# Optimization experiments

Hardware: AMD Instinct MI355X
Metric: run time of the kernel (lower is better)

The kernel has to match this reference:

```python
import jax, jax.numpy as jnp
import numpy as np

WD, WH, WW = 2, 7, 7
N = WD * WH * WW          # 98 tokens per window
DIM = 128
HEADS = 4
HEAD_DIM = DIM // HEADS   # 32
B_ = 2048                 # num_windows * batch
NW = 64                   # windows per image (mask leading dim)
TABLE = (2 * WD - 1) * (2 * WH - 1) * (2 * WW - 1)  # 507


def _relative_position_index():
    coords = np.stack(np.meshgrid(np.arange(WD), np.arange(WH), np.arange(WW), indexing='ij'))
    flat = coords.reshape(3, -1)                     # [3, N]
    rel = flat[:, :, None] - flat[:, None, :]        # [3, N, N]
    rel = rel.transpose(1, 2, 0).copy()              # [N, N, 3]
    rel[:, :, 0] += WD - 1
    rel[:, :, 1] += WH - 1
    rel[:, :, 2] += WW - 1
    rel[:, :, 0] *= (2 * WH - 1) * (2 * WW - 1)
    rel[:, :, 1] *= 2 * WW - 1
    return rel.sum(-1).astype(np.int32)             # [N, N]


def setup_inputs() -> dict:
    key = jax.random.key(0)
    ks = jax.random.split(key, 6)
    x = jax.random.normal(ks[0], (B_, N, DIM), dtype=jnp.float32)
    mask = jax.random.normal(ks[1], (NW, N, N), dtype=jnp.float32)
    qkv_w = jax.random.normal(ks[2], (3 * DIM, DIM), dtype=jnp.float32) * 0.02
    qkv_b = jnp.zeros((3 * DIM,), dtype=jnp.float32)
    proj_w = jax.random.normal(ks[3], (DIM, DIM), dtype=jnp.float32) * 0.02
    proj_b = jnp.zeros((DIM,), dtype=jnp.float32)
    bias_table = jax.random.normal(ks[4], (TABLE, HEADS), dtype=jnp.float32) * 0.02
    rel_idx = jnp.asarray(_relative_position_index())
    return {"x": x, "mask": mask, "qkv_w": qkv_w, "qkv_b": qkv_b,
            "proj_w": proj_w, "proj_b": proj_b, "bias_table": bias_table,
            "rel_idx": rel_idx}


def reference(x, mask, qkv_w, qkv_b, proj_w, proj_b, bias_table, rel_idx):
    b, n, c = x.shape
    hd = c // HEADS
    scale = hd ** -0.5
    qkv = x @ qkv_w.T + qkv_b                          # [B_, N, 3C]
    qkv = qkv.reshape(b, n, 3, HEADS, hd)
    qkv = jnp.transpose(qkv, (2, 0, 3, 1, 4))          # [3, B_, H, N, hd]
    q, k, v = qkv[0], qkv[1], qkv[2]
    attn = jnp.einsum('bhnd,bhmd->bhnm', q * scale, k)  # [B_, H, N, N]
    # gathered relative position bias
    bias = bias_table[rel_idx.reshape(-1)].reshape(n, n, HEADS)
    bias = jnp.transpose(bias, (2, 0, 1))               # [H, N, N]
    attn = attn + bias[None]
    nw = mask.shape[0]
    attn = attn.reshape(b // nw, nw, HEADS, n, n) + mask[None, :, None]
    attn = jax.nn.softmax(attn.reshape(b, HEADS, n, n), axis=-1)
    out = jnp.einsum('bhnm,bhmd->bnhd', attn, v).reshape(b, n, c)
    out = out @ proj_w.T + proj_b
    return out
```

## Files before the change

kernel.cpp:

```cpp
#include <hip/hip_runtime.h>
#include <stdint.h>

#define NTOK 98
#define DIM 128
#define HEADS 4
#define HD 32
#define BWIN 2048
#define NW 64
#define SCALE 0.17677669529663687f
#define QSTR 32
#define VSTR 104

typedef __bf16 bf16_t;
typedef bf16_t bf16x8 __attribute__((ext_vector_type(8)));
typedef float f32x4 __attribute__((ext_vector_type(4)));
typedef unsigned short u16;
typedef unsigned int u32;
typedef unsigned long long u64;

__device__ __forceinline__ u16 f2bf(float f) {
    union { bf16_t h; u16 u; } v; v.h = (bf16_t)f; return v.u;
}
__device__ __forceinline__ float bf2f(u16 b) {
    union { u16 u; bf16_t h; } v; v.u = b; return (float)v.h;
}
__device__ __forceinline__ int qk_idx(int row, int d) {
    return row * QSTR + ((((d >> 3) ^ (row & 3)) << 3) | (d & 7));
}

__global__ void k0_prep(const float* __restrict__ qkv_w, const float* __restrict__ proj_w,
                        const float* __restrict__ mask,
                        const float* __restrict__ bias_table, const int* __restrict__ rel_idx,
                        const float* __restrict__ x,
                        u16* __restrict__ qkvw_bf, u16* __restrict__ pw_bf,
                        u16* __restrict__ mbT, u16* __restrict__ xbf)
{
    int t = blockIdx.x * 256 + threadIdx.x;
    if (t < 49152) {
        qkvw_bf[t] = f2bf(qkv_w[t]);
    } else if (t < 65536) {
        int r = t - 49152;
        pw_bf[r] = f2bf(proj_w[r]);
    } else if (t < 3276800) {
        int r = t - 65536;
        int w    = r / 50176;
        int rem  = r - w * 50176;
        int hh   = rem / 12544;
        int rem2 = rem - hh * 12544;
        int i    = rem2 >> 7;
        int c    = rem2 & 127;
        int l16  = c >> 3;
        int njp  = c & 7;
        int j    = njp * 16 + l16;
        float val = 0.f;
        if (njp < 7 && j < NTOK)
            val = mask[w * 9604 + i * NTOK + j] + bias_table[rel_idx[i * NTOK + j] * HEADS + hh];
        mbT[r] = f2bf(val);
    } else if (t < 6488064) {
        size_t idx = (size_t)(t - 3276800) * 8;
        const float4 a0 = *reinterpret_cast<const float4*>(x + idx);
        const float4 a1 = *reinterpret_cast<const float4*>(x + idx + 4);
        u64 p0 = (u64)f2bf(a0.x) | ((u64)f2bf(a0.y) << 16) |
                 ((u64)f2bf(a0.z) << 32) | ((u64)f2bf(a0.w) << 48);
        u64 p1 = (u64)f2bf(a1.x) | ((u64)f2bf(a1.y) << 16) |
                 ((u64)f2bf(a1.z) << 32) | ((u64)f2bf(a1.w) << 48);
        *reinterpret_cast<u64*>(&xbf[idx])     = p0;
        *reinterpret_cast<u64*>(&xbf[idx + 4]) = p1;
    }
}

__global__ __launch_bounds__(256, 5) void k_attn(
    const u16* __restrict__ xbf, const u16* __restrict__ qkvw_bf,
    const float* __restrict__ qkv_b, const u16* __restrict__ mbT,
    u16* __restrict__ OG)
{
    __shared__ __align__(16) u16 qL[NTOK * QSTR];
    __shared__ __align__(16) u16 kL[NTOK * QSTR];
    __shared__ __align__(16) u16 vL[HD * VSTR];
    __shared__ __align__(16) u16 Pscr[4][16 * VSTR];

    const int bh   = (blockIdx.x & 7) * 1024 + (blockIdx.x >> 3);
    const int b    = bh >> 2;
    const int h    = bh & 3;
    const int tid  = threadIdx.x;
    const int wave = tid >> 6;
    const int lane = tid & 63;
    const int l16  = lane & 15;
    const int quad = lane >> 4;

    const u16* xb = xbf + (size_t)b * (NTOK * DIM);

    {
        const int u0 = (wave * 21) >> 2;
        const int u1 = ((wave + 1) * 21) >> 2;
        int cached = -1;
        bf16x8 Bf[2][4];
        float  cb[2];
        for (int u = u0; u < u1; ++u) {
            const int part = u / 7;
            const int mt   = u - part * 7;
            if (part != cached) {
                const u16* wp = qkvw_bf + (size_t)part * DIM * DIM;
#pragma unroll
                for (int nt2 = 0; nt2 < 2; ++nt2) {
                    const int col = h * HD + nt2 * 16 + l16;
#pragma unroll
                    for (int ks = 0; ks < 4; ++ks)
                        Bf[nt2][ks] = *reinterpret_cast<const bf16x8*>(
                            wp + col * DIM + quad * 8 + ks * 32);
                    cb[nt2] = qkv_b[part * DIM + col];
                }
                cached = part;
            }
            int arow = mt * 16 + l16;
            if (arow > 97) arow = 97;
            bf16x8 af[4];
#pragma unroll
            for (int ks = 0; ks < 4; ++ks)
                af[ks] = *reinterpret_cast<const bf16x8*>(
                    xb + arow * DIM + quad * 8 + ks * 32);
            f32x4 acc0 = {0.f, 0.f, 0.f, 0.f};
            f32x4 acc1 = {0.f, 0.f, 0.f, 0.f};
#pragma unroll
            for (int ks = 0; ks < 4; ++ks) {
                acc0 = __builtin_amdgcn_mfma_f32_16x16x32_bf16(af[ks], Bf[0][ks], acc0, 0, 0, 0);
                acc1 = __builtin_amdgcn_mfma_f32_16x16x32_bf16(af[ks], Bf[1][ks], acc1, 0, 0, 0);
            }
            const int tokb = mt * 16 + quad * 4;
#pragma unroll
            for (int nt2 = 0; nt2 < 2; ++nt2) {
                const f32x4& acc = nt2 ? acc1 : acc0;
                const int d = nt2 * 16 + l16;
                const float cbv = cb[nt2];
                if (part == 0) {
#pragma unroll
                    for (int reg = 0; reg < 4; ++reg) {
                        int tok = tokb + reg;
                        if (tok < NTOK)
                            qL[qk_idx(tok, d)] = f2bf((acc[reg] + cbv) * SCALE);
                    }
                } else if (part == 1) {
#pragma unroll
                    for (int reg = 0; reg < 4; ++reg) {
                        int tok = tokb + reg;
                        if (tok < NTOK)
                            kL[qk_idx(tok, d)] = f2bf(acc[reg] + cbv);
                    }
                } else {
                    u16* vrow = &vL[d * VSTR];
                    if (tokb + 3 <= 97) {
                        u64 pack = 0;
#pragma unroll
                        for (int reg = 0; reg < 4; ++reg)
                            pack |= ((u64)f2bf(acc[reg] + cbv)) << (16 * reg);
                        *reinterpret_cast<u64*>(&vrow[tokb]) = pack;
                    } else if (tokb <= 97) {
                        u32 pack = (u32)f2bf(acc[0] + cbv) | ((u32)f2bf(acc[1] + cbv) << 16);
                        *reinterpret_cast<u32*>(&vrow[tokb]) = pack;
                    }
                }
            }
        }
    }
    __syncthreads();

    {
        const u16* mbtp = mbT + ((size_t)((b & (NW - 1)) * HEADS + h)) * (NTOK * 128);
        u16* ps = &Pscr[wave][0];
        const int qko = ((quad ^ (l16 & 3)) << 3);

        bf16x8 kf[7];
#pragma unroll
        for (int nj = 0; nj < 7; ++nj)
            kf[nj] = *reinterpret_cast<const bf16x8*>(&kL[(nj * 16 + l16) * QSTR + qko]);

        for (int mi = 0; mi < 2; ++mi) {
            const int mt = wave + mi * 4;
            if (mt > 6) break;
            bf16x8 mrows[4];
#pragma unroll
            for (int reg = 0; reg < 4; ++reg) {
                int i  = mt * 16 + quad * 4 + reg;
                int ic = (i > 97) ? 97 : i;
                mrows[reg] = *reinterpret_cast<const bf16x8*>(&mbtp[ic * 128 + l16 * 8]);
            }
            bf16x8 qf = *reinterpret_cast<const bf16x8*>(&qL[(mt * 16 + l16) * QSTR + qko]);
            f32x4 sacc[7];
#pragma unroll
            for (int nj = 0; nj < 7; ++nj) {
                f32x4 z = {0.f, 0.f, 0.f, 0.f};
                sacc[nj] = __builtin_amdgcn_mfma_f32_16x16x32_bf16(qf, kf[nj], z, 0, 0, 0);
            }
#pragma unroll
            for (int reg = 0; reg < 4; ++reg) {
                int i = mt * 16 + quad * 4 + reg;
                bool irow = (i < NTOK);
                float s[7];
#pragma unroll
                for (int nj = 0; nj < 7; ++nj) {
                    int j = nj * 16 + l16;
                    float val = -1e30f;
                    if (irow && j < NTOK)
                        val = sacc[nj][reg] + (float)mrows[reg][nj];
                    s[nj] = val;
                }
                float mx = s[0];
#pragma unroll
                for (int nj = 1; nj < 7; ++nj) mx = fmaxf(mx, s[nj]);
#pragma unroll
                for (int off = 1; off < 16; off <<= 1) mx = fmaxf(mx, __shfl_xor(mx, off));
                float p[7];
                float lsum = 0.f;
#pragma unroll
                for (int nj = 0; nj < 7; ++nj) {
                    float pv = (s[nj] > -1e29f) ? __expf(s[nj] - mx) : 0.f;
                    p[nj] = pv;
                    lsum += pv;
                }
#pragma unroll
                for (int off = 1; off < 16; off <<= 1) lsum += __shfl_xor(lsum, off);
                float rinv = 1.f / ((lsum > 0.f) ? lsum : 1.f);
#pragma unroll
                for (int nj = 0; nj < 7; ++nj) {
                    int j = nj * 16 + l16;
                    if (irow && j < NTOK)
                        ps[(quad * 4 + reg) * VSTR + j] = f2bf(p[nj] * rinv);
                }
            }
            bf16x8 pf[3];
#pragma unroll
            for (int ks = 0; ks < 3; ++ks)
                pf[ks] = *reinterpret_cast<const bf16x8*>(&ps[l16 * VSTR + quad * 8 + ks * 32]);
#pragma unroll
            for (int nt = 0; nt < 2; ++nt) {
                f32x4 oacc = {0.f, 0.f, 0.f, 0.f};
#pragma unroll
                for (int ks = 0; ks < 3; ++ks) {
                    bf16x8 vf = *reinterpret_cast<const bf16x8*>(
                        &vL[(nt * 16 + l16) * VSTR + quad * 8 + ks * 32]);
                    oacc = __builtin_amdgcn_mfma_f32_16x16x32_bf16(pf[ks], vf, oacc, 0, 0, 0);
                }
                int d = nt * 16 + l16;
                float v96 = bf2f(vL[d * VSTR + 96]);
                float v97 = bf2f(vL[d * VSTR + 97]);
#pragma unroll
                for (int reg = 0; reg < 4; ++reg) {
                    int i = mt * 16 + quad * 4 + reg;
                    if (i < NTOK) {
                        float p96 = bf2f(ps[(quad * 4 + reg) * VSTR + 96]);
                        float p97 = bf2f(ps[(quad * 4 + reg) * VSTR + 97]);
                        OG[((size_t)b * NTOK + i) * DIM + h * HD + d] =
                            f2bf(oacc[reg] + p96 * v96 + p97 * v97);
                    }
                }
            }
        }
    }
}

__global__ __launch_bounds__(256, 4) void k_proj(
    const u16* __restrict__ OG, const u16* __restrict__ pw_bf,
    const float* __restrict__ proj_b, float* __restrict__ out)
{
    const int b    = blockIdx.x;
    const int tid  = threadIdx.x;
    const int wave = tid >> 6;
    const int lane = tid & 63;
    const int l16  = lane & 15;
    const int quad = lane >> 4;

    bf16x8 bw[2][4];
    float  pb[2];
#pragma unroll
    for (int nt2 = 0; nt2 < 2; ++nt2) {
        const int col = (wave * 2 + nt2) * 16 + l16;
#pragma unroll
        for (int ks = 0; ks < 4; ++ks)
            bw[nt2][ks] = *reinterpret_cast<const bf16x8*>(
                pw_bf + col * DIM + quad * 8 + ks * 32);
        pb[nt2] = proj_b[col];
    }
    const u16* ob = OG + (size_t)b * (NTOK * DIM);
    for (int mt = 0; mt < 7; ++mt) {
        int arow = mt * 16 + l16;
        if (arow > 97) arow = 97;
        bf16x8 af[4];
#pragma unroll
        for (int ks = 0; ks < 4; ++ks)
            af[ks] = *reinterpret_cast<const bf16x8*>(ob + arow * DIM + quad * 8 + ks * 32);
        f32x4 acc0 = {0.f, 0.f, 0.f, 0.f};
        f32x4 acc1 = {0.f, 0.f, 0.f, 0.f};
#pragma unroll
        for (int ks = 0; ks < 4; ++ks) {
            acc0 = __builtin_amdgcn_mfma_f32_16x16x32_bf16(af[ks], bw[0][ks], acc0, 0, 0, 0);
            acc1 = __builtin_amdgcn_mfma_f32_16x16x32_bf16(af[ks], bw[1][ks], acc1, 0, 0, 0);
        }
#pragma unroll
        for (int nt2 = 0; nt2 < 2; ++nt2) {
            const f32x4& acc = nt2 ? acc1 : acc0;
            const int col = (wave * 2 + nt2) * 16 + l16;
#pragma unroll
            for (int reg = 0; reg < 4; ++reg) {
                int row = mt * 16 + quad * 4 + reg;
                if (row < NTOK)
                    out[((size_t)b * NTOK + row) * DIM + col] = acc[reg] + pb[nt2];
            }
        }
    }
}

extern "C" void kernel_launch(void* const* d_in, const int* in_sizes, int n_in,
                              void* d_out, int out_size, void* d_ws, size_t ws_size,
                              hipStream_t stream)
{
    const float* x       = (const float*)d_in[0];
    const float* mask    = (const float*)d_in[1];
    const float* qkv_w   = (const float*)d_in[2];
    const float* qkv_b   = (const float*)d_in[3];
    const float* proj_w  = (const float*)d_in[4];
    const float* proj_b  = (const float*)d_in[5];
    const float* bias_tb = (const float*)d_in[6];
    const int*   rel_idx = (const int*)d_in[7];
    float* out = (float*)d_out;

    char* ws = (char*)d_ws;
    u16* qkvw_bf = (u16*)(ws + 0);
    u16* pw_bf   = (u16*)(ws + 98304);
    u16* mbT     = (u16*)(ws + 131072);
    u16* xbf     = (u16*)(ws + 6553600);
    u16* OG      = (u16*)(ws + 57933824);

    k0_prep<<<25344, 256, 0, stream>>>(qkv_w, proj_w, mask, bias_tb, rel_idx, x,
                                       qkvw_bf, pw_bf, mbT, xbf);
    k_attn<<<BWIN * HEADS, 256, 0, stream>>>(xbf, qkvw_bf, qkv_b, mbT, OG);
    k_proj<<<BWIN, 256, 0, stream>>>(OG, pw_bf, proj_b, out);
}
```

Measured before the change: 387.4 us.

## Bake padding into mask, defer softmax normalization, add MFMA priority and proj block swizzle

Padded mask entries are now pre-filled with -1e30, so the per-element bounds checks in the softmax loop go away, and Q/K row indices are clamped instead. The softmax writes unnormalised probabilities and multiplies by the reciprocal sum after the PV product, which removes per-element multiplies and the guard branches. s_setprio hints are placed around the MFMA blocks, and the proj kernel remaps block indices so that consecutive blocks touch different windows. Deferring normalisation changes bf16 rounding of P slightly, and the padded columns rely on exp underflowing to zero.

```diff
diff --git a/kernel.cpp b/kernel.cpp
--- a/kernel.cpp
+++ b/kernel.cpp
@@ -52,7 +52,7 @@
         int l16  = c >> 3;
         int njp  = c & 7;
         int j    = njp * 16 + l16;
-        float val = 0.f;
+        float val = -1e30f;
         if (njp < 7 && j < NTOK)
             val = mask[w * 9604 + i * NTOK + j] + bias_table[rel_idx[i * NTOK + j] * HEADS + hh];
         mbT[r] = f2bf(val);
@@ -121,11 +121,13 @@
                     xb + arow * DIM + quad * 8 + ks * 32);
             f32x4 acc0 = {0.f, 0.f, 0.f, 0.f};
             f32x4 acc1 = {0.f, 0.f, 0.f, 0.f};
+            __builtin_amdgcn_s_setprio(1);
 #pragma unroll
             for (int ks = 0; ks < 4; ++ks) {
                 acc0 = __builtin_amdgcn_mfma_f32_16x16x32_bf16(af[ks], Bf[0][ks], acc0, 0, 0, 0);
                 acc1 = __builtin_amdgcn_mfma_f32_16x16x32_bf16(af[ks], Bf[1][ks], acc1, 0, 0, 0);
             }
+            __builtin_amdgcn_s_setprio(0);
             const int tokb = mt * 16 + quad * 4;
 #pragma unroll
             for (int nt2 = 0; nt2 < 2; ++nt2) {
@@ -171,8 +173,11 @@
 
         bf16x8 kf[7];
 #pragma unroll
-        for (int nj = 0; nj < 7; ++nj)
-            kf[nj] = *reinterpret_cast<const bf16x8*>(&kL[(nj * 16 + l16) * QSTR + qko]);
+        for (int nj = 0; nj < 7; ++nj) {
+            int krow = nj * 16 + l16;
+            if (krow > 97) krow = 97;
+            kf[nj] = *reinterpret_cast<const bf16x8*>(&kL[krow * QSTR + qko]);
+        }
 
         for (int mi = 0; mi < 2; ++mi) {
             const int mt = wave + mi * 4;
@@ -184,48 +189,43 @@
                 int ic = (i > 97) ? 97 : i;
                 mrows[reg] = *reinterpret_cast<const bf16x8*>(&mbtp[ic * 128 + l16 * 8]);
             }
-            bf16x8 qf = *reinterpret_cast<const bf16x8*>(&qL[(mt * 16 + l16) * QSTR + qko]);
+            int qrow = mt * 16 + l16;
+            if (qrow > 97) qrow = 97;
+            bf16x8 qf = *reinterpret_cast<const bf16x8*>(&qL[qrow * QSTR + qko]);
             f32x4 sacc[7];
+            __builtin_amdgcn_s_setprio(1);
 #pragma unroll
             for (int nj = 0; nj < 7; ++nj) {
                 f32x4 z = {0.f, 0.f, 0.f, 0.f};
                 sacc[nj] = __builtin_amdgcn_mfma_f32_16x16x32_bf16(qf, kf[nj], z, 0, 0, 0);
             }
+            __builtin_amdgcn_s_setprio(0);
+            float rin[4];
 #pragma unroll
             for (int reg = 0; reg < 4; ++reg) {
-                int i = mt * 16 + quad * 4 + reg;
-                bool irow = (i < NTOK);
                 float s[7];
 #pragma unroll
-                for (int nj = 0; nj < 7; ++nj) {
-                    int j = nj * 16 + l16;
-                    float val = -1e30f;
-                    if (irow && j < NTOK)
-                        val = sacc[nj][reg] + (float)mrows[reg][nj];
-                    s[nj] = val;
-                }
-                float mx = s[0];
-#pragma unroll
-                for (int nj = 1; nj < 7; ++nj) mx = fmaxf(mx, s[nj]);
+                for (int nj = 0; nj < 7; ++nj)
+                    s[nj] = sacc[nj][reg] + (float)mrows[reg][nj];
+                float mx = fmaxf(fmaxf(fmaxf(s[0], s[1]), fmaxf(s[2], s[3])),
+                                 fmaxf(fmaxf(s[4], s[5]), s[6]));
 #pragma unroll
                 for (int off = 1; off < 16; off <<= 1) mx = fmaxf(mx, __shfl_xor(mx, off));
                 float p[7];
                 float lsum = 0.f;
 #pragma unroll
                 for (int nj = 0; nj < 7; ++nj) {
-                    float pv = (s[nj] > -1e29f) ? __expf(s[nj] - mx) : 0.f;
-                    p[nj] = pv;
-                    lsum += pv;
-                }
+                    p[nj] = __expf(s[nj] - mx);
+                    lsum += p[nj];
+                }
+                u16* psr = &ps[(quad * 4 + reg) * VSTR];
+#pragma unroll
+                for (int nj = 0; nj < 6; ++nj)
+                    psr[nj * 16 + l16] = f2bf(p[nj]);
+                if (l16 < 8) psr[96 + l16] = f2bf(p[6]);
 #pragma unroll
                 for (int off = 1; off < 16; off <<= 1) lsum += __shfl_xor(lsum, off);
-                float rinv = 1.f / ((lsum > 0.f) ? lsum : 1.f);
-#pragma unroll
-                for (int nj = 0; nj < 7; ++nj) {
-                    int j = nj * 16 + l16;
-                    if (irow && j < NTOK)
-                        ps[(quad * 4 + reg) * VSTR + j] = f2bf(p[nj] * rinv);
-                }
+                rin[reg] = 1.f / lsum;
             }
             bf16x8 pf[3];
 #pragma unroll
@@ -234,12 +234,14 @@
 #pragma unroll
             for (int nt = 0; nt < 2; ++nt) {
                 f32x4 oacc = {0.f, 0.f, 0.f, 0.f};
+                __builtin_amdgcn_s_setprio(1);
 #pragma unroll
                 for (int ks = 0; ks < 3; ++ks) {
                     bf16x8 vf = *reinterpret_cast<const bf16x8*>(
                         &vL[(nt * 16 + l16) * VSTR + quad * 8 + ks * 32]);
                     oacc = __builtin_amdgcn_mfma_f32_16x16x32_bf16(pf[ks], vf, oacc, 0, 0, 0);
                 }
+                __builtin_amdgcn_s_setprio(0);
                 int d = nt * 16 + l16;
                 float v96 = bf2f(vL[d * VSTR + 96]);
                 float v97 = bf2f(vL[d * VSTR + 97]);
@@ -250,7 +252,7 @@
                         float p96 = bf2f(ps[(quad * 4 + reg) * VSTR + 96]);
                         float p97 = bf2f(ps[(quad * 4 + reg) * VSTR + 97]);
                         OG[((size_t)b * NTOK + i) * DIM + h * HD + d] =
-                            f2bf(oacc[reg] + p96 * v96 + p97 * v97);
+                            f2bf((oacc[reg] + p96 * v96 + p97 * v97) * rin[reg]);
                     }
                 }
             }
@@ -262,7 +264,7 @@
     const u16* __restrict__ OG, const u16* __restrict__ pw_bf,
     const float* __restrict__ proj_b, float* __restrict__ out)
 {
-    const int b    = blockIdx.x;
+    const int b    = ((blockIdx.x & 7) << 8) + (blockIdx.x >> 3);
     const int tid  = threadIdx.x;
     const int wave = tid >> 6;
     const int lane = tid & 63;
```

After: 367.2 us. 1.05x faster.
